# Performance work log

Hardware: AMD Instinct MI355X
Metric: run time of the kernel (lower is better)

Reference implementation:

```python
import jax, jax.numpy as jnp
import numpy as np

N_NODES = 50000
N_EDGES = 800000
D_IN = 128
D_HID = 128
D_OUT = 128


def _sage_conv(x, row, col, Wl, Wr, b):
    # PyG SAGEConv (mean aggregation, root weight, bias):
    # out = mean_{j in N(i)} x_j @ Wl^T + x_i @ Wr^T + b
    n = x.shape[0]
    msg = x[col]                                            # [E, D] gather from source nodes
    agg = jax.ops.segment_sum(msg, row, num_segments=n)     # [N, D]
    deg = jax.ops.segment_sum(jnp.ones((row.shape[0],), x.dtype), row, num_segments=n)
    agg = agg / jnp.maximum(deg, 1.0)[:, None]
    return agg @ Wl.T + x @ Wr.T + b


def setup_inputs() -> dict:
    key = jax.random.key(0)
    ks = jax.random.split(key, 12)
    x = jax.random.normal(ks[0], (N_NODES, D_IN), dtype=jnp.float32)
    edge_row = jax.random.randint(ks[1], (N_EDGES,), 0, N_NODES)
    edge_col = jax.random.randint(ks[2], (N_EDGES,), 0, N_NODES)
    dims = [(D_HID, D_IN), (D_HID, D_HID), (D_OUT, D_HID)]
    inp = {"x": x, "edge_row": edge_row, "edge_col": edge_col}
    for i, (do, di) in enumerate(dims):
        s = 1.0 / np.sqrt(di)
        inp[f"Wl{i}"] = jax.random.uniform(ks[3 + 3 * i], (do, di), jnp.float32, -s, s)
        inp[f"Wr{i}"] = jax.random.uniform(ks[4 + 3 * i], (do, di), jnp.float32, -s, s)
        inp[f"b{i}"] = jax.random.uniform(ks[5 + 3 * i], (do,), jnp.float32, -s, s)
    return inp


def reference(x, edge_row, edge_col, Wl0, Wr0, b0, Wl1, Wr1, b1, Wl2, Wr2, b2):
    # Single branch (num_layers=[3]), use_res=True, dropout=0 (eval mode).
    params = [(Wl0, Wr0, b0), (Wl1, Wr1, b1), (Wl2, Wr2, b2)]
    x1 = _sage_conv(x, edge_row, edge_col, *params[0])
    for Wl, Wr, b in params[1:]:
        x2 = x1
        x1 = jax.nn.relu(x1)
        x1 = _sage_conv(x1, edge_row, edge_col, Wl, Wr, b) + x2
    # x_final = sum(branches) / number; one branch -> divide by 1
    return x1 / 1.0
```

## Files before the change

kernel.cpp:

```cpp
#include <hip/hip_runtime.h>

#define NN 50000
#define NE 800000
#define D  128

typedef _Float16 f16;
typedef _Float16 f16x4 __attribute__((ext_vector_type(4)));
typedef _Float16 f16x8 __attribute__((ext_vector_type(8)));
typedef float f32x4 __attribute__((ext_vector_type(4)));
typedef float f32x2 __attribute__((ext_vector_type(2)));
typedef unsigned short u16;
typedef unsigned int u32;
typedef unsigned char u8;

__global__ __launch_bounds__(256) void prep(
    const float* __restrict__ x, f16* __restrict__ xf, u8* __restrict__ xf8,
    const float* w0, const float* w1, const float* w2,
    const float* w3, const float* w4, const float* w5,
    f16* d0, f16* d1, f16* d2, f16* d3, f16* d4, f16* d5,
    int* __restrict__ deg) {
    int b = blockIdx.x;
    if (b < 6250) {
        int i = b * 256 + threadIdx.x;
        float4 v = ((const float4*)x)[i];
        f16x4 o = {(f16)v.x, (f16)v.y, (f16)v.z, (f16)v.w};
        ((f16x4*)xf)[i] = o;
        u32 lo = __builtin_amdgcn_cvt_pk_fp8_f32(v.x, v.y, 0, false);
        u32 pk = __builtin_amdgcn_cvt_pk_fp8_f32(v.z, v.w, lo, true);
        ((u32*)xf8)[i] = pk;
    } else if (b < 6346) {
        int wb = b - 6250;
        int mat = wb >> 4;
        const float* s; f16* d;
        switch (mat) {
            case 0: s = w0; d = d0; break; case 1: s = w1; d = d1; break;
            case 2: s = w2; d = d2; break; case 3: s = w3; d = d3; break;
            case 4: s = w4; d = d4; break; default: s = w5; d = d5; break;
        }
        int i = (wb & 15) * 256 + threadIdx.x;
        float4 v = ((const float4*)s)[i];
        f16x4 o = {(f16)v.x, (f16)v.y, (f16)v.z, (f16)v.w};
        ((f16x4*)d)[i] = o;
    } else {
        int i = (b - 6346) * 256 + threadIdx.x;
        if (i < NN) deg[i] = 0;
    }
}


__global__ __launch_bounds__(256) void count_deg_rank(
    const int* __restrict__ row, int* __restrict__ deg, u16* __restrict__ rank, int e2) {
    int i = blockIdx.x * blockDim.x + threadIdx.x;
    if (i < e2) {
        int2 r = ((const int2*)row)[i];
        unsigned ra = (unsigned)atomicAdd(&deg[r.x], 1);
        unsigned rb = (unsigned)atomicAdd(&deg[r.y], 1);
        ((unsigned*)rank)[i] = (ra & 0xffffu) | (rb << 16);
    }
}

__global__ void scan_offsets(const int* __restrict__ deg, int* __restrict__ offsets, int n) {
    __shared__ int s[1024];
    int lim = blockIdx.x << 10;
    int a = 0;
    for (int i = threadIdx.x; i < lim; i += 1024) a += deg[i];
    s[threadIdx.x] = a;
    __syncthreads();
    for (int off = 512; off > 0; off >>= 1) {
        if (threadIdx.x < off) s[threadIdx.x] += s[threadIdx.x + off];
        __syncthreads();
    }
    int base = s[0];
    __syncthreads();
    int i = lim + threadIdx.x;
    int dv = (i < n) ? deg[i] : 0;
    s[threadIdx.x] = dv;
    __syncthreads();
    for (int off = 1; off < 1024; off <<= 1) {
        int t = (threadIdx.x >= (unsigned)off) ? s[threadIdx.x - off] : 0;
        __syncthreads();
        s[threadIdx.x] += t;
        __syncthreads();
    }
    if (i < n) {
        offsets[i + 1] = s[threadIdx.x] + base;
        if (i == 0) offsets[0] = 0;
    }
}

__global__ __launch_bounds__(256) void fill_csr(
    const int* __restrict__ row, const int* __restrict__ col,
    const u16* __restrict__ rank, const int* __restrict__ offsets,
    u16* __restrict__ csr_col, int e2) {
    int i = blockIdx.x * blockDim.x + threadIdx.x;
    if (i < e2) {
        int2 r = ((const int2*)row)[i];
        int2 c = ((const int2*)col)[i];
        unsigned rk = ((const unsigned*)rank)[i];
        csr_col[offsets[r.x] + (int)(rk & 0xffffu)] = (u16)c.x;
        csr_col[offsets[r.y] + (int)(rk >> 16)]     = (u16)c.y;
    }
}

__global__ __launch_bounds__(256) void aggregate_f8(
    const u8* __restrict__ h8, const int* __restrict__ offsets,
    const u16* __restrict__ csr, f16* __restrict__ agg) {
    int node = blockIdx.x * 4 + (threadIdx.x >> 6);
    int lane = threadIdx.x & 63;
    int sub = lane >> 4, fl = lane & 15;
    int s0 = offsets[node], e0 = offsets[node + 1];
    int deg = e0 - s0;

    float acc[8];
#pragma unroll
    for (int u = 0; u < 8; ++u) acc[u] = 0.f;

    const u8* hp = h8 + fl * 8;

#define UNPACK_ADD(w)                                                  \
    do {                                                               \
        f32x2 p;                                                       \
        p = __builtin_amdgcn_cvt_pk_f32_fp8((w).x, false);             \
        acc[0] += p.x; acc[1] += p.y;                                  \
        p = __builtin_amdgcn_cvt_pk_f32_fp8((w).x, true);              \
        acc[2] += p.x; acc[3] += p.y;                                  \
        p = __builtin_amdgcn_cvt_pk_f32_fp8((w).y, false);             \
        acc[4] += p.x; acc[5] += p.y;                                  \
        p = __builtin_amdgcn_cvt_pk_f32_fp8((w).y, true);              \
        acc[6] += p.x; acc[7] += p.y;                                  \
    } while (0)

    int j = s0 + sub;
    for (int it = deg >> 3; it > 0; --it, j += 8) {
        int c0 = (int)csr[j];
        int c1 = (int)csr[j + 4];
        uint2 w0 = *(const uint2*)(hp + (size_t)c0 * D);
        uint2 w1 = *(const uint2*)(hp + (size_t)c1 * D);
        UNPACK_ADD(w0);
        UNPACK_ADD(w1);
    }
    if (deg & 4) {
        int c = (int)csr[j];
        uint2 w = *(const uint2*)(hp + (size_t)c * D);
        UNPACK_ADD(w);
        j += 4;
    }
    if (sub < (deg & 3)) {
        int c = (int)csr[j];
        uint2 w = *(const uint2*)(hp + (size_t)c * D);
        UNPACK_ADD(w);
    }
#undef UNPACK_ADD

#pragma unroll
    for (int u = 0; u < 8; ++u) {
        acc[u] += __shfl_xor(acc[u], 16, 64);
        acc[u] += __shfl_xor(acc[u], 32, 64);
    }
    if (sub == 0) {
        float inv = 1.f / fmaxf((float)deg, 1.f);
        f16x8 o;
#pragma unroll
        for (int u = 0; u < 8; ++u) o[u] = (f16)(acc[u] * inv);
        *((f16x8*)(agg + (size_t)node * D) + fl) = o;
    }
}

#define WPAD 72

template<int RELU_X, int ADD_RES, int OUT_F32>
__global__ __launch_bounds__(256, 4) void sage_gemm_mfma(
    const f16* __restrict__ aggb, const f16* __restrict__ xb,
    const f16* __restrict__ Wl, const f16* __restrict__ Wr,
    const float* __restrict__ bias, float* __restrict__ outf,
    f16* __restrict__ outh, u8* __restrict__ out8) {
    __shared__ f16 sW[2][128][WPAD];

    const int tid  = threadIdx.x;
    const int wave = tid >> 6;
    const int lane = tid & 63;
    const int lm = lane & 15;
    const int q  = lane >> 4;
    const int mt = blockIdx.x * 64 + wave * 16;

    int row = mt + lm;
    int rclamp = (row < NN) ? row : NN - 1;

    f16x8 Aa[4], Ax[4];
    const f16* arow = aggb + (size_t)rclamp * D + q * 8;
    const f16* xrow = xb  + (size_t)rclamp * D + q * 8;
#pragma unroll
    for (int ks = 0; ks < 4; ++ks) {
        Aa[ks] = *(const f16x8*)(arow + ks * 32);
        f16x8 v = *(const f16x8*)(xrow + ks * 32);
        if (RELU_X) {
#pragma unroll
            for (int u = 0; u < 8; ++u) v[u] = (v[u] < (f16)0) ? (f16)0 : v[u];
        }
        Ax[ks] = v;
    }

    f32x4 acc[8];
#pragma unroll
    for (int nt = 0; nt < 8; ++nt) acc[nt] = (f32x4){0.f, 0.f, 0.f, 0.f};

    for (int p = 0; p < 2; ++p) {
        __syncthreads();
#pragma unroll
        for (int it = 0; it < 8; ++it) {
            int idx = tid + it * 256;
            int mat = idx >> 10;
            int n   = (idx >> 3) & 127;
            int c   = idx & 7;
            const f16* W = mat ? Wr : Wl;
            f16x8 v = *(const f16x8*)(W + n * D + p * 64 + c * 8);
            *(f16x8*)&sW[mat][n][c * 8] = v;
        }
        __syncthreads();

#pragma unroll
        for (int nt = 0; nt < 8; ++nt) {
#pragma unroll
            for (int k2 = 0; k2 < 2; ++k2) {
                f16x8 bl = *(const f16x8*)&sW[0][nt * 16 + lm][k2 * 32 + q * 8];
                acc[nt] = __builtin_amdgcn_mfma_f32_16x16x32_f16(Aa[p * 2 + k2], bl, acc[nt], 0, 0, 0);
                f16x8 br = *(const f16x8*)&sW[1][nt * 16 + lm][k2 * 32 + q * 8];
                acc[nt] = __builtin_amdgcn_mfma_f32_16x16x32_f16(Ax[p * 2 + k2], br, acc[nt], 0, 0, 0);
            }
        }
    }

#pragma unroll
    for (int nt = 0; nt < 8; ++nt) {
        int n = nt * 16 + lm;
        float bval = bias[n];
#pragma unroll
        for (int r = 0; r < 4; ++r) {
            int m = mt + q * 4 + r;
            if (m < NN) {
                size_t idx = (size_t)m * D + n;
                float v = acc[nt][r] + bval;
                if (ADD_RES) v += (float)xb[idx];
                if (OUT_F32) {
                    outf[idx] = v;
                } else {
                    outh[idx] = (f16)v;
                    u32 t = __builtin_amdgcn_cvt_pk_fp8_f32(fmaxf(v, 0.f), 0.f, 0, false);
                    out8[idx] = (u8)(t & 0xffu);
                }
            }
        }
    }
}


extern "C" void kernel_launch(void* const* d_in, const int* in_sizes, int n_in,
                              void* d_out, int out_size, void* d_ws, size_t ws_size,
                              hipStream_t stream) {
    const float* x    = (const float*)d_in[0];
    const int*   erow = (const int*)d_in[1];
    const int*   ecol = (const int*)d_in[2];
    const float* Wl0 = (const float*)d_in[3];
    const float* Wr0 = (const float*)d_in[4];
    const float* b0  = (const float*)d_in[5];
    const float* Wl1 = (const float*)d_in[6];
    const float* Wr1 = (const float*)d_in[7];
    const float* b1  = (const float*)d_in[8];
    const float* Wl2 = (const float*)d_in[9];
    const float* Wr2 = (const float*)d_in[10];
    const float* b2  = (const float*)d_in[11];

    char* ws = (char*)d_ws;
    size_t off = 0;
    auto carve = [&](size_t bytes) -> void* {
        void* p = ws + off;
        off = (off + bytes + 255) & ~(size_t)255;
        return p;
    };
    int*   deg     = (int*)carve((size_t)NN * 4);
    int*   offsets = (int*)carve((size_t)(NN + 1) * 4);
    u16*   rank    = (u16*)carve((size_t)NE * 2);
    u16*   csr_col = (u16*)carve((size_t)NE * 2);
    f16*   xf      = (f16*)carve((size_t)NN * D * 2);
    f16*   x1      = (f16*)carve((size_t)NN * D * 2);
    f16*   aggb    = (f16*)carve((size_t)NN * D * 2);
    u8*    xf8     = (u8*)carve((size_t)NN * D);
    u8*    x1f8    = (u8*)carve((size_t)NN * D);
    f16*   wl0 = (f16*)carve(D * D * 2); f16* wr0 = (f16*)carve(D * D * 2);
    f16*   wl1 = (f16*)carve(D * D * 2); f16* wr1 = (f16*)carve(D * D * 2);
    f16*   wl2 = (f16*)carve(D * D * 2); f16* wr2 = (f16*)carve(D * D * 2);
    (void)ws_size; (void)in_sizes; (void)n_in; (void)out_size;

    float* outp = (float*)d_out;

    prep<<<6542, 256, 0, stream>>>(x, xf, xf8, Wl0, Wr0, Wl1, Wr1, Wl2, Wr2,
                                   wl0, wr0, wl1, wr1, wl2, wr2, deg);

    const int e2 = NE / 2;
    count_deg_rank<<<(e2 + 255) / 256, 256, 0, stream>>>(erow, deg, rank, e2);
    scan_offsets<<<(NN + 1023) / 1024, 1024, 0, stream>>>(deg, offsets, NN);
    fill_csr<<<(e2 + 255) / 256, 256, 0, stream>>>(erow, ecol, rank, offsets, csr_col, e2);

    const int agrid = NN / 4;
    const int ggrid = (NN + 63) / 64;

    aggregate_f8<<<agrid, 256, 0, stream>>>(xf8, offsets, csr_col, aggb);
    sage_gemm_mfma<0, 0, 0><<<ggrid, 256, 0, stream>>>(aggb, xf, wl0, wr0, b0,
                                                       nullptr, x1, x1f8);
    aggregate_f8<<<agrid, 256, 0, stream>>>(x1f8, offsets, csr_col, aggb);
    sage_gemm_mfma<1, 1, 0><<<ggrid, 256, 0, stream>>>(aggb, x1, wl1, wr1, b1,
                                                       nullptr, x1, x1f8);
    aggregate_f8<<<agrid, 256, 0, stream>>>(x1f8, offsets, csr_col, aggb);
    sage_gemm_mfma<1, 1, 1><<<ggrid, 256, 0, stream>>>(aggb, x1, wl2, wr2, b2,
                                                       outp, nullptr, nullptr);
}
```

Baseline: 282.9 us.

## Fuse degree counting into prep, pack fp8 accumulation, shrink GEMM LDS tile

Degree counting and rank assignment move into the prep kernel, and the deg array is zeroed with a memset instead of extra prep blocks, which saves one kernel launch. The aggregation accumulates into packed float2 vectors so the compiler can use packed adds. The GEMM stages one 128x64 weight slice at a time instead of two, halving LDS use to allow higher occupancy, at the cost of four barrier phases instead of two.

After: 283.5 us. About the same (+0.2%).

```diff
diff --git a/kernel.cpp b/kernel.cpp
--- a/kernel.cpp
+++ b/kernel.cpp
@@ -18,7 +18,8 @@
     const float* w0, const float* w1, const float* w2,
     const float* w3, const float* w4, const float* w5,
     f16* d0, f16* d1, f16* d2, f16* d3, f16* d4, f16* d5,
-    int* __restrict__ deg) {
+    const int* __restrict__ erow, int* __restrict__ deg, u16* __restrict__ rank,
+    int e2) {
     int b = blockIdx.x;
     if (b < 6250) {
         int i = b * 256 + threadIdx.x;
@@ -43,19 +44,12 @@
         ((f16x4*)d)[i] = o;
     } else {
         int i = (b - 6346) * 256 + threadIdx.x;
-        if (i < NN) deg[i] = 0;
-    }
-}
-
-
-__global__ __launch_bounds__(256) void count_deg_rank(
-    const int* __restrict__ row, int* __restrict__ deg, u16* __restrict__ rank, int e2) {
-    int i = blockIdx.x * blockDim.x + threadIdx.x;
-    if (i < e2) {
-        int2 r = ((const int2*)row)[i];
-        unsigned ra = (unsigned)atomicAdd(&deg[r.x], 1);
-        unsigned rb = (unsigned)atomicAdd(&deg[r.y], 1);
-        ((unsigned*)rank)[i] = (ra & 0xffffu) | (rb << 16);
+        if (i < e2) {
+            int2 r = ((const int2*)erow)[i];
+            unsigned ra = (unsigned)atomicAdd(&deg[r.x], 1);
+            unsigned rb = (unsigned)atomicAdd(&deg[r.y], 1);
+            ((unsigned*)rank)[i] = (ra & 0xffffu) | (rb << 16);
+        }
     }
 }
 
@@ -111,23 +105,18 @@
     int s0 = offsets[node], e0 = offsets[node + 1];
     int deg = e0 - s0;
 
-    float acc[8];
-#pragma unroll
-    for (int u = 0; u < 8; ++u) acc[u] = 0.f;
+    f32x2 acc2[4];
+#pragma unroll
+    for (int u = 0; u < 4; ++u) acc2[u] = (f32x2){0.f, 0.f};
 
     const u8* hp = h8 + fl * 8;
 
 #define UNPACK_ADD(w)                                                  \
     do {                                                               \
-        f32x2 p;                                                       \
-        p = __builtin_amdgcn_cvt_pk_f32_fp8((w).x, false);             \
-        acc[0] += p.x; acc[1] += p.y;                                  \
-        p = __builtin_amdgcn_cvt_pk_f32_fp8((w).x, true);              \
-        acc[2] += p.x; acc[3] += p.y;                                  \
-        p = __builtin_amdgcn_cvt_pk_f32_fp8((w).y, false);             \
-        acc[4] += p.x; acc[5] += p.y;                                  \
-        p = __builtin_amdgcn_cvt_pk_f32_fp8((w).y, true);              \
-        acc[6] += p.x; acc[7] += p.y;                                  \
+        acc2[0] += __builtin_amdgcn_cvt_pk_f32_fp8((w).x, false);      \
+        acc2[1] += __builtin_amdgcn_cvt_pk_f32_fp8((w).x, true);       \
+        acc2[2] += __builtin_amdgcn_cvt_pk_f32_fp8((w).y, false);      \
+        acc2[3] += __builtin_amdgcn_cvt_pk_f32_fp8((w).y, true);       \
     } while (0)
 
     int j = s0 + sub;
@@ -153,15 +142,20 @@
 #undef UNPACK_ADD
 
 #pragma unroll
-    for (int u = 0; u < 8; ++u) {
-        acc[u] += __shfl_xor(acc[u], 16, 64);
-        acc[u] += __shfl_xor(acc[u], 32, 64);
+    for (int u = 0; u < 4; ++u) {
+        acc2[u].x += __shfl_xor(acc2[u].x, 16, 64);
+        acc2[u].y += __shfl_xor(acc2[u].y, 16, 64);
+        acc2[u].x += __shfl_xor(acc2[u].x, 32, 64);
+        acc2[u].y += __shfl_xor(acc2[u].y, 32, 64);
     }
     if (sub == 0) {
         float inv = 1.f / fmaxf((float)deg, 1.f);
         f16x8 o;
 #pragma unroll
-        for (int u = 0; u < 8; ++u) o[u] = (f16)(acc[u] * inv);
+        for (int u = 0; u < 4; ++u) {
+            o[2 * u]     = (f16)(acc2[u].x * inv);
+            o[2 * u + 1] = (f16)(acc2[u].y * inv);
+        }
         *((f16x8*)(agg + (size_t)node * D) + fl) = o;
     }
 }
@@ -174,7 +168,7 @@
     const f16* __restrict__ Wl, const f16* __restrict__ Wr,
     const float* __restrict__ bias, float* __restrict__ outf,
     f16* __restrict__ outh, u8* __restrict__ out8) {
-    __shared__ f16 sW[2][128][WPAD];
+    __shared__ f16 sW[128][WPAD];
 
     const int tid  = threadIdx.x;
     const int wave = tid >> 6;
@@ -204,28 +198,27 @@
 #pragma unroll
     for (int nt = 0; nt < 8; ++nt) acc[nt] = (f32x4){0.f, 0.f, 0.f, 0.f};
 
-    for (int p = 0; p < 2; ++p) {
+#pragma unroll
+    for (int s = 0; s < 4; ++s) {
+        const int mat = s & 1;
+        const int kh  = s >> 1;
+        if (s) __syncthreads();
+#pragma unroll
+        for (int it = 0; it < 4; ++it) {
+            int idx = tid + it * 256;
+            int n = idx >> 3, c = idx & 7;
+            const f16* W = mat ? Wr : Wl;
+            *(f16x8*)&sW[n][c * 8] = *(const f16x8*)(W + n * D + kh * 64 + c * 8);
+        }
         __syncthreads();
-#pragma unroll
-        for (int it = 0; it < 8; ++it) {
-            int idx = tid + it * 256;
-            int mat = idx >> 10;
-            int n   = (idx >> 3) & 127;
-            int c   = idx & 7;
-            const f16* W = mat ? Wr : Wl;
-            f16x8 v = *(const f16x8*)(W + n * D + p * 64 + c * 8);
-            *(f16x8*)&sW[mat][n][c * 8] = v;
-        }
-        __syncthreads();
 
 #pragma unroll
         for (int nt = 0; nt < 8; ++nt) {
 #pragma unroll
             for (int k2 = 0; k2 < 2; ++k2) {
-                f16x8 bl = *(const f16x8*)&sW[0][nt * 16 + lm][k2 * 32 + q * 8];
-                acc[nt] = __builtin_amdgcn_mfma_f32_16x16x32_f16(Aa[p * 2 + k2], bl, acc[nt], 0, 0, 0);
-                f16x8 br = *(const f16x8*)&sW[1][nt * 16 + lm][k2 * 32 + q * 8];
-                acc[nt] = __builtin_amdgcn_mfma_f32_16x16x32_f16(Ax[p * 2 + k2], br, acc[nt], 0, 0, 0);
+                f16x8 bm = *(const f16x8*)&sW[nt * 16 + lm][k2 * 32 + q * 8];
+                f16x8 af = mat ? Ax[kh * 2 + k2] : Aa[kh * 2 + k2];
+                acc[nt] = __builtin_amdgcn_mfma_f32_16x16x32_f16(af, bm, acc[nt], 0, 0, 0);
             }
         }
     }
@@ -293,11 +286,13 @@
 
     float* outp = (float*)d_out;
 
-    prep<<<6542, 256, 0, stream>>>(x, xf, xf8, Wl0, Wr0, Wl1, Wr1, Wl2, Wr2,
-                                   wl0, wr0, wl1, wr1, wl2, wr2, deg);
-
     const int e2 = NE / 2;
-    count_deg_rank<<<(e2 + 255) / 256, 256, 0, stream>>>(erow, deg, rank, e2);
+
+    hipMemsetAsync(deg, 0, (size_t)NN * 4, stream);
+    prep<<<7909, 256, 0, stream>>>(x, xf, xf8, Wl0, Wr0, Wl1, Wr1, Wl2, Wr2,
+                                   wl0, wr0, wl1, wr1, wl2, wr2,
+                                   erow, deg, rank, e2);
+
     scan_offsets<<<(NN + 1023) / 1024, 1024, 0, stream>>>(deg, offsets, NN);
     fill_csr<<<(e2 + 255) / 256, 256, 0, stream>>>(erow, ecol, rank, offsets, csr_col, e2);
 
```
